# Kernel optimization log

Measured on AMD Instinct MI355X. Metric: run time of the kernel, lower is better.

## Reference

```python
import jax, jax.numpy as jnp
import numpy as np

N = 2048            # matrix dimension (d_model-sized orthogonal factor)
BATCH = 8192        # number of row-vectors multiplied by the matrix exponential
SIGN = 1            # slogdet sign; 1 means no row negation
TRANSPOSE = False
N_FLAT = N * (N - 1) // 2


def setup_inputs() -> dict:
    key = jax.random.key(0)
    k1, k2 = jax.random.split(key)
    X = jax.random.normal(k1, (BATCH, N), dtype=jnp.float32)
    # small scale keeps the 9-term Taylor series well inside its convergence regime
    S_flat = jax.random.normal(k2, (N_FLAT,), dtype=jnp.float32) * 0.01
    return {"X": X, "S_flat": S_flat}


def _weight(S_flat):
    # unfold: scatter strict upper triangle, antisymmetrize
    rows, cols = jnp.triu_indices(N, k=1)
    M = jnp.zeros((N, N), dtype=S_flat.dtype).at[rows, cols].set(S_flat)
    S = M - M.T
    # truncated Taylor series exp(S) = I + S + S^2/2! + ... + S^9/9!
    T = S
    Q = jnp.eye(N, dtype=S.dtype) + S
    for i in range(2, 10):
        T = (T @ S) / i
        Q = Q + T
    if SIGN == -1:
        if TRANSPOSE:
            Q = Q.at[:, 0].multiply(-1.0)
        else:
            Q = Q.at[0].multiply(-1.0)
    return Q


def reference(X, S_flat):
    return X @ _weight(S_flat)
```

## Files before the change

### kernel.cpp

```cpp
#include <hip/hip_runtime.h>
#include <hip/hip_bf16.h>
#include <stdint.h>

#define N_DIM 2048
#define BATCH_SZ 8192

typedef __bf16 bf16;
typedef __bf16 bf16x4 __attribute__((ext_vector_type(4)));
typedef __bf16 bf16x8 __attribute__((ext_vector_type(8)));
typedef float f32x4 __attribute__((ext_vector_type(4)));

__device__ __forceinline__ void gld16(const bf16* g, bf16* l) {
  __builtin_amdgcn_global_load_lds(
      (const __attribute__((address_space(1))) void*)g,
      (__attribute__((address_space(3))) void*)l, 16, 0, 0);
}

__global__ __launch_bounds__(256) void unfold_t(const float* __restrict__ Sflat,
                                                bf16* __restrict__ Wb,
                                                bf16* __restrict__ Wtb) {
  const int bi = blockIdx.y;
  const int bj = blockIdx.x;
  if (bi > bj) return;
  __shared__ float U[64][65];
  const int t  = threadIdx.x;
  const int c  = t & 63;
  const int r0 = t >> 6;

#pragma unroll
  for (int k = 0; k < 16; ++k) {
    const int r = k * 4 + r0;
    const int i = bi * 64 + r;
    const int j = bj * 64 + c;
    float v = 0.0f;
    if (i < j) {
      const int fi = i * (N_DIM - 1) - ((i * (i - 1)) >> 1) + (j - i - 1);
      v = Sflat[fi];
    }
    U[r][c] = v;
  }
  __syncthreads();

  if (bi == bj) {
#pragma unroll
    for (int k = 0; k < 16; ++k) {
      const int r = k * 4 + r0;
      const float s = U[r][c] - U[c][r];
      const size_t idx = (size_t)(bi * 64 + r) * N_DIM + bj * 64 + c;
      Wb[idx]  = (bf16)(-s);
      Wtb[idx] = (bf16)( s);
    }
  } else {
#pragma unroll
    for (int k = 0; k < 16; ++k) {
      const int r = k * 4 + r0;
      const float u = U[r][c];
      const size_t idx = (size_t)(bi * 64 + r) * N_DIM + bj * 64 + c;
      Wb[idx]  = (bf16)(-u);
      Wtb[idx] = (bf16)( u);
      const float um = U[c][r];
      const size_t idm = (size_t)(bj * 64 + r) * N_DIM + bi * 64 + c;
      Wb[idm]  = (bf16)( um);
      Wtb[idm] = (bf16)(-um);
    }
  }
}

__global__ void cast_kernel(const float* __restrict__ in, bf16* __restrict__ out) {
  int t = blockIdx.x * blockDim.x + threadIdx.x;
  float4 v = ((const float4*)in)[t];
  bf16x4 o;
  o.x = (bf16)v.x; o.y = (bf16)v.y; o.z = (bf16)v.z; o.w = (bf16)v.w;
  ((bf16x4*)out)[t] = o;
}

template <int MODE>
__global__ __launch_bounds__(256, 2) void gemm_w(
    const bf16* __restrict__ A, const bf16* __restrict__ Bt,
    bf16* __restrict__ O1, bf16* __restrict__ O2,
    const bf16* __restrict__ Wb, int M, int N, int K) {
  __shared__ __align__(16) bf16 As[3 * 2 * 64 * 32];
  __shared__ __align__(16) bf16 Bs[3 * 2 * 128 * 32];

  const int tid  = threadIdx.x;
  const int lane = tid & 63;
  const int wave = tid >> 6;
  const int wr   = wave >> 1;
  const int wc   = wave & 1;
  const int quad = lane >> 4;
  const int l16  = lane & 15;

  const int nwg    = gridDim.x * gridDim.y;
  const int linear = blockIdx.y * gridDim.x + blockIdx.x;
  const int wg = (linear & 7) * (nwg >> 3) + (linear >> 3);
  const int bx = wg & 15;
  const int by = wg >> 4;
  const int m0 = by * 64;
  const int n0 = bx * 128;

  const int srow  = lane >> 2;
  const int sslot = (lane & 3) ^ ((lane >> 3) & 3);
  const bf16* gA  = A  + (size_t)(m0 + wave * 16 + srow) * K + sslot * 8;
  const bf16* gB1 = Bt + (size_t)(n0 + wave * 16 + srow) * K + sslot * 8;
  const bf16* gB2 = gB1 + (size_t)64 * K;
  bf16* lA  = As + wave * 512;
  bf16* lB1 = Bs + wave * 512;
  bf16* lB2 = Bs + wave * 512 + 2048;

  const int NS = K >> 6;

  auto STAGE = [&](int t, int s) {
#pragma unroll
    for (int k = 0; k < 2; ++k) {
      const size_t ko = (size_t)t * 64 + k * 32;
      gld16(gA  + ko, lA  + (s * 2 + k) * 2048);
      gld16(gB1 + ko, lB1 + (s * 2 + k) * 4096);
      gld16(gB2 + ko, lB2 + (s * 2 + k) * 4096);
    }
  };

  STAGE(0, 0);
  STAGE(1, 1);
  asm volatile("s_waitcnt vmcnt(6)" ::: "memory");
  __builtin_amdgcn_sched_barrier(0);
  __builtin_amdgcn_s_barrier();
  __builtin_amdgcn_sched_barrier(0);

  f32x4 acc[2][4] = {};
  const int rswz = (quad ^ ((l16 >> 1) & 3)) * 8;
  const int arow = wr * 32 + l16;
  const int brow = wc * 64 + l16;

  auto body = [&](int t, int s) {
    if (t + 2 < NS) STAGE(t + 2, (s + 2) % 3);
    bf16x8 af[2][2], bfr[2][4];
#pragma unroll
    for (int k = 0; k < 2; ++k) {
      const bf16* ab = As + (s * 2 + k) * 2048;
      const bf16* bb = Bs + (s * 2 + k) * 4096;
#pragma unroll
      for (int mi = 0; mi < 2; ++mi)
        af[k][mi] = *(const bf16x8*)&ab[(arow + mi * 16) * 32 + rswz];
#pragma unroll
      for (int ni = 0; ni < 4; ++ni)
        bfr[k][ni] = *(const bf16x8*)&bb[(brow + ni * 16) * 32 + rswz];
    }
    __builtin_amdgcn_s_setprio(1);
#pragma unroll
    for (int k = 0; k < 2; ++k)
#pragma unroll
      for (int mi = 0; mi < 2; ++mi)
#pragma unroll
        for (int ni = 0; ni < 4; ++ni)
          acc[mi][ni] = __builtin_amdgcn_mfma_f32_16x16x32_bf16(
              af[k][mi], bfr[k][ni], acc[mi][ni], 0, 0, 0);
    __builtin_amdgcn_s_setprio(0);
    if (t < NS - 1) {
      if (t + 2 < NS)
        asm volatile("s_waitcnt vmcnt(6)" ::: "memory");
      else
        asm volatile("s_waitcnt vmcnt(0)" ::: "memory");
      __builtin_amdgcn_sched_barrier(0);
      __builtin_amdgcn_s_barrier();
      __builtin_amdgcn_sched_barrier(0);
    }
  };

  const int NS3 = NS - (NS % 3);
#pragma unroll 1
  for (int t0 = 0; t0 < NS3; t0 += 3) {
    body(t0, 0);
    body(t0 + 1, 1);
    body(t0 + 2, 2);
  }
#pragma unroll
  for (int u = 0; u < 3; ++u) {
    const int t = NS3 + u;
    if (t < NS) body(t, u);
  }

#pragma unroll
  for (int mi = 0; mi < 2; ++mi) {
    const int r0 = m0 + wr * 32 + mi * 16 + quad * 4;
#pragma unroll
    for (int ni = 0; ni < 4; ++ni) {
      const int col = n0 + wc * 64 + ni * 16 + l16;
#pragma unroll
      for (int r = 0; r < 4; ++r) {
        const int row = r0 + r;
        const size_t idx = (size_t)row * N + col;
        const float v = acc[mi][ni][r];
        if (MODE == 1) {
          O1[idx] = (bf16)v;
          const float w = (float)Wb[idx];
          const float d = (row == col) ? 1.0f : 0.0f;
          O2[idx] = (bf16)(0.5f * d - (1.0f / 6.0f) * w + (1.0f / 24.0f) * v);
        } else {
          const float w = (float)Wb[idx];
          const float d = (row == col) ? 1.0f : 0.0f;
          O1[idx] = (bf16)(v + d + w);
        }
      }
    }
  }
}

__global__ __launch_bounds__(512, 2) void gemm256(
    const bf16* __restrict__ A, const bf16* __restrict__ Bt,
    float* __restrict__ Cf, int M, int N, int K) {
  __shared__ __align__(16) bf16 As[4 * 256 * 32];
  __shared__ __align__(16) bf16 Bs[4 * 256 * 32];

  const int tid  = threadIdx.x;
  const int lane = tid & 63;
  const int wave = tid >> 6;
  const int wr   = wave >> 2;
  const int wc   = wave & 3;
  const int quad = lane >> 4;
  const int l16  = lane & 15;

  const int nwg    = gridDim.x * gridDim.y;
  const int linear = blockIdx.y * gridDim.x + blockIdx.x;
  const int wg = (linear & 7) * (nwg >> 3) + (linear >> 3);
  const int bx = wg & 7;
  const int by = wg >> 3;
  const int m0 = by * 256;
  const int n0 = bx * 256;

  const int srow  = lane >> 2;
  const int sslot = (lane & 3) ^ ((lane >> 3) & 3);
  const bf16* pA1 = A  + (size_t)(m0 + wave * 16 + srow) * K + sslot * 8;
  const bf16* pA2 = pA1 + (size_t)128 * K;
  const bf16* pB1 = Bt + (size_t)(n0 + wave * 16 + srow) * K + sslot * 8;
  const bf16* pB2 = pB1 + (size_t)128 * K;
  bf16* lA1 = As + wave * 512;
  bf16* lA2 = As + wave * 512 + 4096;
  bf16* lB1 = Bs + wave * 512;
  bf16* lB2 = Bs + wave * 512 + 4096;

  const int NT = K >> 5;

#pragma unroll
  for (int tt = 0; tt < 3; ++tt) {
    gld16(pA1 + tt * 32, lA1 + tt * 8192);
    gld16(pA2 + tt * 32, lA2 + tt * 8192);
    gld16(pB1 + tt * 32, lB1 + tt * 8192);
    gld16(pB2 + tt * 32, lB2 + tt * 8192);
  }
  asm volatile("s_waitcnt vmcnt(8)" ::: "memory");
  __builtin_amdgcn_s_barrier();
  __builtin_amdgcn_sched_barrier(0);

  f32x4 acc[8][4] = {};
  const int rswz = (quad ^ ((l16 >> 1) & 3)) * 8;
  const int arow = wr * 128 + l16;
  const int brow = wc * 64 + l16;

  size_t kpre = 96;

#pragma unroll 1
  for (int t4 = 0; t4 < NT; t4 += 4) {
#pragma unroll
    for (int u = 0; u < 4; ++u) {
      const int t = t4 + u;
      if (t + 3 < NT) {
        const int b = (u + 3) & 3;
        const size_t ko = kpre + (size_t)u * 32;
        gld16(pA1 + ko, lA1 + b * 8192);
        gld16(pA2 + ko, lA2 + b * 8192);
        gld16(pB1 + ko, lB1 + b * 8192);
        gld16(pB2 + ko, lB2 + b * 8192);
      }
      const bf16* ab = As + u * 8192;
      const bf16* bb = Bs + u * 8192;
      bf16x8 af[8], bfr[4];
#pragma unroll
      for (int mi = 0; mi < 8; ++mi)
        af[mi] = *(const bf16x8*)&ab[(arow + mi * 16) * 32 + rswz];
#pragma unroll
      for (int ni = 0; ni < 4; ++ni)
        bfr[ni] = *(const bf16x8*)&bb[(brow + ni * 16) * 32 + rswz];
      __builtin_amdgcn_s_setprio(1);
#pragma unroll
      for (int mi = 0; mi < 8; ++mi)
#pragma unroll
        for (int ni = 0; ni < 4; ++ni)
          acc[mi][ni] = __builtin_amdgcn_mfma_f32_16x16x32_bf16(
              af[mi], bfr[ni], acc[mi][ni], 0, 0, 0);
      __builtin_amdgcn_s_setprio(0);
      if (t < NT - 1) {
        if (t < NT - 3)
          asm volatile("s_waitcnt vmcnt(8)" ::: "memory");
        else if (t == NT - 3)
          asm volatile("s_waitcnt vmcnt(4)" ::: "memory");
        else
          asm volatile("s_waitcnt vmcnt(0)" ::: "memory");
        __builtin_amdgcn_sched_barrier(0);
        __builtin_amdgcn_s_barrier();
        __builtin_amdgcn_sched_barrier(0);
      }
    }
    kpre += 128;
  }

#pragma unroll
  for (int mi = 0; mi < 8; ++mi) {
    const int r0 = m0 + wr * 128 + mi * 16 + quad * 4;
#pragma unroll
    for (int ni = 0; ni < 4; ++ni) {
      const int col = n0 + wc * 64 + ni * 16 + l16;
#pragma unroll
      for (int r = 0; r < 4; ++r)
        Cf[(size_t)(r0 + r) * N + col] = acc[mi][ni][r];
    }
  }
}

extern "C" void kernel_launch(void* const* d_in, const int* in_sizes, int n_in,
                              void* d_out, int out_size, void* d_ws, size_t ws_size,
                              hipStream_t stream) {
  const float* X     = (const float*)d_in[0];
  const float* Sflat = (const float*)d_in[1];
  float* out = (float*)d_out;
  char* ws = (char*)d_ws;

  bf16* Xb   = (bf16*)(ws);
  bf16* Wb   = (bf16*)(ws + (32u << 20));
  bf16* Wtb  = (bf16*)(ws + (40u << 20));
  bf16* W2b  = (bf16*)(ws + (48u << 20));
  bf16* Btm  = (bf16*)(ws + (56u << 20));
  bf16* Qtb  = (bf16*)(ws + (64u << 20));

  unfold_t<<<dim3(32, 32), 256, 0, stream>>>(Sflat, Wb, Wtb);
  cast_kernel<<<(BATCH_SZ * N_DIM / 4) / 256, 256, 0, stream>>>(X, Xb);

  const dim3 gW(N_DIM / 128, N_DIM / 64);
  gemm_w<1><<<gW, 256, 0, stream>>>(Wb, Wtb, W2b, Btm, Wb,
                                    N_DIM, N_DIM, N_DIM);
  gemm_w<2><<<gW, 256, 0, stream>>>(W2b, Btm, Qtb, nullptr, Wb,
                                    N_DIM, N_DIM, N_DIM);
  gemm256<<<dim3(N_DIM / 256, BATCH_SZ / 256), 512, 0, stream>>>(
      Xb, Qtb, out, BATCH_SZ, N_DIM, N_DIM);
}
```

Before: 262.0 us.

## Fuse two weight GEMMs into one persistent kernel with grid-wide barrier

The two separate 64x128-tile weight GEMM launches become one 256-block kernel with 128x128 tiles and 512 threads. The phases are separated by an atomic-counter grid barrier that reuses the output buffer as the counter, zeroed by a memset. Its pipeline is now double-buffered over 128-wide K chunks. This is meant to remove a launch gap and tail effect between the dependent GEMMs, but it relies on all 256 blocks being co-resident and drops to one block per CU.

```diff
diff --git a/kernel.cpp b/kernel.cpp
--- a/kernel.cpp
+++ b/kernel.cpp
@@ -75,120 +75,93 @@
 }
 
 template <int MODE>
-__global__ __launch_bounds__(256, 2) void gemm_w(
+__device__ __forceinline__ void gemm128_phase(
     const bf16* __restrict__ A, const bf16* __restrict__ Bt,
     bf16* __restrict__ O1, bf16* __restrict__ O2,
-    const bf16* __restrict__ Wb, int M, int N, int K) {
-  __shared__ __align__(16) bf16 As[3 * 2 * 64 * 32];
-  __shared__ __align__(16) bf16 Bs[3 * 2 * 128 * 32];
-
+    const bf16* __restrict__ Wb, bf16* As, bf16* Bs, int m0, int n0) {
+  constexpr int K  = N_DIM;
+  constexpr int NP = K >> 7;
   const int tid  = threadIdx.x;
   const int lane = tid & 63;
   const int wave = tid >> 6;
-  const int wr   = wave >> 1;
-  const int wc   = wave & 1;
+  const int wr   = wave >> 2;
+  const int wc   = wave & 3;
   const int quad = lane >> 4;
   const int l16  = lane & 15;
 
-  const int nwg    = gridDim.x * gridDim.y;
-  const int linear = blockIdx.y * gridDim.x + blockIdx.x;
-  const int wg = (linear & 7) * (nwg >> 3) + (linear >> 3);
-  const int bx = wg & 15;
-  const int by = wg >> 4;
-  const int m0 = by * 64;
-  const int n0 = bx * 128;
-
   const int srow  = lane >> 2;
   const int sslot = (lane & 3) ^ ((lane >> 3) & 3);
-  const bf16* gA  = A  + (size_t)(m0 + wave * 16 + srow) * K + sslot * 8;
-  const bf16* gB1 = Bt + (size_t)(n0 + wave * 16 + srow) * K + sslot * 8;
-  const bf16* gB2 = gB1 + (size_t)64 * K;
-  bf16* lA  = As + wave * 512;
-  bf16* lB1 = Bs + wave * 512;
-  bf16* lB2 = Bs + wave * 512 + 2048;
-
-  const int NS = K >> 6;
-
-  auto STAGE = [&](int t, int s) {
-#pragma unroll
-    for (int k = 0; k < 2; ++k) {
-      const size_t ko = (size_t)t * 64 + k * 32;
-      gld16(gA  + ko, lA  + (s * 2 + k) * 2048);
-      gld16(gB1 + ko, lB1 + (s * 2 + k) * 4096);
-      gld16(gB2 + ko, lB2 + (s * 2 + k) * 4096);
-    }
-  };
-
-  STAGE(0, 0);
-  STAGE(1, 1);
-  asm volatile("s_waitcnt vmcnt(6)" ::: "memory");
+  const bf16* gA = A  + (size_t)(m0 + wave * 16 + srow) * K + sslot * 8;
+  const bf16* gB = Bt + (size_t)(n0 + wave * 16 + srow) * K + sslot * 8;
+  bf16* lA = As + wave * 512;
+  bf16* lB = Bs + wave * 512;
+
+#pragma unroll
+  for (int k = 0; k < 4; ++k) {
+    gld16(gA + k * 32, lA + k * 4096);
+    gld16(gB + k * 32, lB + k * 4096);
+  }
+  asm volatile("s_waitcnt vmcnt(0)" ::: "memory");
   __builtin_amdgcn_sched_barrier(0);
   __builtin_amdgcn_s_barrier();
   __builtin_amdgcn_sched_barrier(0);
 
-  f32x4 acc[2][4] = {};
+  f32x4 acc[4][2] = {};
   const int rswz = (quad ^ ((l16 >> 1) & 3)) * 8;
-  const int arow = wr * 32 + l16;
-  const int brow = wc * 64 + l16;
-
-  auto body = [&](int t, int s) {
-    if (t + 2 < NS) STAGE(t + 2, (s + 2) % 3);
-    bf16x8 af[2][2], bfr[2][4];
-#pragma unroll
-    for (int k = 0; k < 2; ++k) {
-      const bf16* ab = As + (s * 2 + k) * 2048;
-      const bf16* bb = Bs + (s * 2 + k) * 4096;
-#pragma unroll
-      for (int mi = 0; mi < 2; ++mi)
-        af[k][mi] = *(const bf16x8*)&ab[(arow + mi * 16) * 32 + rswz];
-#pragma unroll
-      for (int ni = 0; ni < 4; ++ni)
-        bfr[k][ni] = *(const bf16x8*)&bb[(brow + ni * 16) * 32 + rswz];
-    }
-    __builtin_amdgcn_s_setprio(1);
-#pragma unroll
-    for (int k = 0; k < 2; ++k)
-#pragma unroll
-      for (int mi = 0; mi < 2; ++mi)
-#pragma unroll
-        for (int ni = 0; ni < 4; ++ni)
+  const int arow = wr * 64 + l16;
+  const int brow = wc * 32 + l16;
+
+#pragma unroll 1
+  for (int t = 0; t < NP; ++t) {
+    if (t + 1 < NP) {
+      const int h = ((t + 1) & 1) * 4;
+      const size_t ko = (size_t)(t + 1) * 128;
+#pragma unroll
+      for (int k = 0; k < 4; ++k) {
+        gld16(gA + ko + k * 32, lA + (h + k) * 4096);
+        gld16(gB + ko + k * 32, lB + (h + k) * 4096);
+      }
+    }
+    __builtin_amdgcn_sched_barrier(0);
+    const int base = (t & 1) * 4;
+#pragma unroll
+    for (int kk = 0; kk < 4; ++kk) {
+      const bf16* ab = As + (base + kk) * 4096;
+      const bf16* bb = Bs + (base + kk) * 4096;
+      bf16x8 af[4], bfr[2];
+#pragma unroll
+      for (int mi = 0; mi < 4; ++mi)
+        af[mi] = *(const bf16x8*)&ab[(arow + mi * 16) * 32 + rswz];
+#pragma unroll
+      for (int ni = 0; ni < 2; ++ni)
+        bfr[ni] = *(const bf16x8*)&bb[(brow + ni * 16) * 32 + rswz];
+      __builtin_amdgcn_s_setprio(1);
+#pragma unroll
+      for (int mi = 0; mi < 4; ++mi)
+#pragma unroll
+        for (int ni = 0; ni < 2; ++ni)
           acc[mi][ni] = __builtin_amdgcn_mfma_f32_16x16x32_bf16(
-              af[k][mi], bfr[k][ni], acc[mi][ni], 0, 0, 0);
-    __builtin_amdgcn_s_setprio(0);
-    if (t < NS - 1) {
-      if (t + 2 < NS)
-        asm volatile("s_waitcnt vmcnt(6)" ::: "memory");
-      else
-        asm volatile("s_waitcnt vmcnt(0)" ::: "memory");
+              af[mi], bfr[ni], acc[mi][ni], 0, 0, 0);
+      __builtin_amdgcn_s_setprio(0);
+    }
+    if (t + 1 < NP) {
+      asm volatile("s_waitcnt vmcnt(0)" ::: "memory");
       __builtin_amdgcn_sched_barrier(0);
       __builtin_amdgcn_s_barrier();
       __builtin_amdgcn_sched_barrier(0);
     }
-  };
-
-  const int NS3 = NS - (NS % 3);
-#pragma unroll 1
-  for (int t0 = 0; t0 < NS3; t0 += 3) {
-    body(t0, 0);
-    body(t0 + 1, 1);
-    body(t0 + 2, 2);
-  }
-#pragma unroll
-  for (int u = 0; u < 3; ++u) {
-    const int t = NS3 + u;
-    if (t < NS) body(t, u);
-  }
-
-#pragma unroll
-  for (int mi = 0; mi < 2; ++mi) {
-    const int r0 = m0 + wr * 32 + mi * 16 + quad * 4;
-#pragma unroll
-    for (int ni = 0; ni < 4; ++ni) {
-      const int col = n0 + wc * 64 + ni * 16 + l16;
+  }
+
+#pragma unroll
+  for (int mi = 0; mi < 4; ++mi) {
+    const int r0 = m0 + wr * 64 + mi * 16 + quad * 4;
+#pragma unroll
+    for (int ni = 0; ni < 2; ++ni) {
+      const int col = n0 + wc * 32 + ni * 16 + l16;
 #pragma unroll
       for (int r = 0; r < 4; ++r) {
         const int row = r0 + r;
-        const size_t idx = (size_t)row * N + col;
+        const size_t idx = (size_t)row * N_DIM + col;
         const float v = acc[mi][ni][r];
         if (MODE == 1) {
           O1[idx] = (bf16)v;
@@ -203,6 +176,34 @@
       }
     }
   }
+}
+
+__global__ __launch_bounds__(512, 1) void wfused(
+    const bf16* __restrict__ Wb, const bf16* __restrict__ Wtb,
+    bf16* __restrict__ W2b, bf16* __restrict__ Btm,
+    bf16* __restrict__ Qtb, unsigned* __restrict__ cnt) {
+  __shared__ __align__(16) bf16 As[8 * 128 * 32];
+  __shared__ __align__(16) bf16 Bs[8 * 128 * 32];
+
+  const int linear = blockIdx.x;
+  const int wg = (linear & 7) * 32 + (linear >> 3);
+  const int m0 = (wg >> 4) * 128;
+  const int n0 = (wg & 15) * 128;
+
+  gemm128_phase<1>(Wb, Wtb, W2b, Btm, Wb, As, Bs, m0, n0);
+
+  __threadfence();
+  __syncthreads();
+  if (threadIdx.x == 0) {
+    __hip_atomic_fetch_add(cnt, 1u, __ATOMIC_ACQ_REL, __HIP_MEMORY_SCOPE_AGENT);
+    while (__hip_atomic_load(cnt, __ATOMIC_ACQUIRE, __HIP_MEMORY_SCOPE_AGENT) <
+           256u)
+      __builtin_amdgcn_s_sleep(8);
+  }
+  __syncthreads();
+  __threadfence();
+
+  gemm128_phase<2>(W2b, Btm, Qtb, nullptr, Wb, As, Bs, m0, n0);
 }
 
 __global__ __launch_bounds__(512, 2) void gemm256(
@@ -331,14 +332,13 @@
   bf16* Btm  = (bf16*)(ws + (56u << 20));
   bf16* Qtb  = (bf16*)(ws + (64u << 20));
 
+  hipMemsetAsync(out, 0, 64, stream);
+
   unfold_t<<<dim3(32, 32), 256, 0, stream>>>(Sflat, Wb, Wtb);
   cast_kernel<<<(BATCH_SZ * N_DIM / 4) / 256, 256, 0, stream>>>(X, Xb);
 
-  const dim3 gW(N_DIM / 128, N_DIM / 64);
-  gemm_w<1><<<gW, 256, 0, stream>>>(Wb, Wtb, W2b, Btm, Wb,
-                                    N_DIM, N_DIM, N_DIM);
-  gemm_w<2><<<gW, 256, 0, stream>>>(W2b, Btm, Qtb, nullptr, Wb,
-                                    N_DIM, N_DIM, N_DIM);
+  wfused<<<256, 512, 0, stream>>>(Wb, Wtb, W2b, Btm, Qtb, (unsigned*)out);
+
   gemm256<<<dim3(N_DIM / 256, BATCH_SZ / 256), 512, 0, stream>>>(
       Xb, Qtb, out, BATCH_SZ, N_DIM, N_DIM);
 }
```

After: 398.5 us. +52.1%, slower.
